# Optimization experiments

Hardware: AMD Instinct MI355X
Metric: run time of the kernel (lower is better)

## Reference

```python
import jax, jax.numpy as jnp
import numpy as np

B, E, F_IN = 8192, 64, 7
D, H = 64, 4           # feature_size, heads
HD = D // H            # features per head


def setup_inputs() -> dict:
    key = jax.random.key(0)
    ks = jax.random.split(key, 14)
    def lin(k, i, o):
        return jax.random.normal(k, (i, o), jnp.float32) * (1.0 / np.sqrt(i))
    return {
        "x": jax.random.normal(ks[0], (B, E, F_IN), jnp.float32),
        # ego embedding MLP (7->64->64, with bias)
        "ego_w0": lin(ks[1], F_IN, D), "ego_b0": jnp.zeros((D,), jnp.float32),
        "ego_w1": lin(ks[2], D, D),    "ego_b1": jnp.zeros((D,), jnp.float32),
        # others embedding MLP (separate weights)
        "oth_w0": lin(ks[3], F_IN, D), "oth_b0": jnp.zeros((D,), jnp.float32),
        "oth_w1": lin(ks[4], D, D),    "oth_b1": jnp.zeros((D,), jnp.float32),
        # attention projections (no bias)
        "Wk": lin(ks[5], D, D), "Wv": lin(ks[6], D, D),
        "Wq": lin(ks[7], D, D), "Wc": lin(ks[8], D, D),
    }


def _mlp(x, w0, b0, w1, b1):
    h = jax.nn.relu(x @ w0 + b0)
    return jax.nn.relu(h @ w1 + b1)


def reference(x, ego_w0, ego_b0, ego_w1, ego_b1,
              oth_w0, oth_b0, oth_w1, oth_b1, Wk, Wv, Wq, Wc):
    b = x.shape[0]
    mask = x[:, :, 0] < 0.5                       # [B, E] absent entities
    ego = _mlp(x[:, 0:1, :], ego_w0, ego_b0, ego_w1, ego_b1)   # [B, 1, D]
    others = _mlp(x[:, 1:, :], oth_w0, oth_b0, oth_w1, oth_b1)  # [B, E-1, D]
    input_all = jnp.concatenate([ego, others], axis=1)          # [B, E, D]

    # project and split heads -> [B, H, E, HD]
    k = (input_all @ Wk).reshape(b, E, H, HD).transpose(0, 2, 1, 3)
    v = (input_all @ Wv).reshape(b, E, H, HD).transpose(0, 2, 1, 3)
    q = (ego @ Wq).reshape(b, 1, H, HD).transpose(0, 2, 1, 3)   # [B, H, 1, HD]

    scores = jnp.einsum('bhqd,bhkd->bhqk', q, k) / np.sqrt(HD)  # [B, H, 1, E]
    scores = jnp.where(mask[:, None, None, :], -1e9, scores)
    p_attn = jax.nn.softmax(scores, axis=-1)
    out = jnp.einsum('bhqk,bhkd->bhqd', p_attn, v)              # [B, H, 1, HD]
    out = out.reshape(b, D)                                      # concat heads
    result = (out @ Wc + ego[:, 0, :]) * 0.5                     # [B, D]
    return result
```

## Files before the change

kernel.cpp:

```cpp
#include <hip/hip_runtime.h>
#include <hip/hip_bf16.h>


typedef __attribute__((ext_vector_type(8))) short short8;
typedef __attribute__((ext_vector_type(4))) short short4b;
typedef __attribute__((ext_vector_type(4))) float f32x4;

#define SY 72

#define LDS_FENCE() asm volatile("s_waitcnt lgkmcnt(0)" ::: "memory")

#define WS_G    0
#define WS_EGW0 16384
#define WS_EGW1 16896
#define WS_WVT  20992
#define WS_WCT  25088
#define WS_W0T  29184
#define WS_W1T  29696

__device__ __forceinline__ short f2bs(float x) {
    __hip_bfloat16 h = __float2bfloat16(x);
    return __builtin_bit_cast(short, h);
}
__device__ __forceinline__ unsigned short f2u(float x) {
    __hip_bfloat16 h = __float2bfloat16(x);
    return __builtin_bit_cast(unsigned short, h);
}
__device__ __forceinline__ short8 ldws8(const unsigned short* p) {
    return *(const short8*)p;
}

__global__ void pack_ws(const float* __restrict__ ego_w0, const float* __restrict__ ego_w1,
                        const float* __restrict__ oth_w0, const float* __restrict__ oth_w1,
                        const float* __restrict__ Wk, const float* __restrict__ Wv,
                        const float* __restrict__ Wq, const float* __restrict__ Wc,
                        unsigned short* __restrict__ ws) {
    const int blk = blockIdx.x, t = threadIdx.x;
    if (blk < 256) {
        const int n = blk, h = n >> 6, f = n & 63, j = t;
        float a = 0.f;
#pragma unroll
        for (int d = 0; d < 16; ++d)
            a = fmaf(Wq[j * 64 + h * 16 + d], Wk[f * 64 + h * 16 + d], a);
        ws[WS_G + n * 64 + j] = f2u(a);
    } else {
        const int n = blk - 256, k = t;
        ws[WS_EGW1 + n * 64 + k] = f2u(ego_w1[k * 64 + n]);
        ws[WS_WVT  + n * 64 + k] = f2u(Wv[k * 64 + n]);
        ws[WS_WCT  + n * 64 + k] = f2u(Wc[k * 64 + n]);
        ws[WS_W1T  + n * 64 + k] = f2u(oth_w1[k * 64 + n]);
        if (k < 8) {
            ws[WS_EGW0 + n * 8 + k] = (k < 7) ? f2u(ego_w0[k * 64 + n]) : 0;
            ws[WS_W0T  + n * 8 + k] = (k < 7) ? f2u(oth_w0[k * 64 + n]) : 0;
        }
    }
}

__global__ __launch_bounds__(64, 2)
void ego_attn_kernel(const float* __restrict__ x,
                     const float* __restrict__ ego_b0, const float* __restrict__ ego_b1,
                     const float* __restrict__ oth_b0, const float* __restrict__ oth_b1,
                     const unsigned short* __restrict__ ws,
                     float* __restrict__ out)
{
    __shared__ __align__(16) short hy[64 * SY];
    __shared__ __align__(16) short kqb[16 * SY];
    __shared__ __align__(16) short pa[4 * SY];
    __shared__ __align__(16) short py[16 * SY];
    __shared__ __align__(16) short xld[4 * 64 * 8];
    __shared__ __align__(16) float egf[4 * 64];
    __shared__ unsigned long long mball[4];

    const int lane = threadIdx.x;
    const int lg = lane >> 4, ln = lane & 15;
    const int gb = blockIdx.x * 4;
    const short8 z8 = {0, 0, 0, 0, 0, 0, 0, 0};

    short8 w0f[4], w1f[2][4];
#pragma unroll
    for (int ct = 0; ct < 4; ++ct)
        w0f[ct] = (lg == 0) ? ldws8(ws + WS_W0T + (ct * 16 + ln) * 8) : z8;
#pragma unroll
    for (int kc = 0; kc < 2; ++kc)
#pragma unroll
        for (int ct = 0; ct < 4; ++ct)
            w1f[kc][ct] = ldws8(ws + WS_W1T + (ct * 16 + ln) * 64 + kc * 32 + lg * 8);
    float b0v[4], b1v[4], eb0v[4], eb1v[4];
#pragma unroll
    for (int ct = 0; ct < 4; ++ct) {
        b0v[ct]  = oth_b0[ct * 16 + ln];
        b1v[ct]  = oth_b1[ct * 16 + ln];
        eb0v[ct] = ego_b0[ct * 16 + ln];
        eb1v[ct] = ego_b1[ct * 16 + ln];
    }

#pragma unroll
    for (int i = 0; i < 4; ++i) {
        const float* xr = x + (size_t)(gb + i) * 448 + lane * 7;
        const float v0 = xr[0];
        const unsigned long long mb = __ballot(v0 < 0.5f);
        if (lane == 0) mball[i] = mb;
        short8 v;
        v[0] = f2bs(v0);
#pragma unroll
        for (int k = 1; k < 7; ++k) v[k] = f2bs(xr[k]);
        v[7] = 0;
        *(short8*)&xld[((i << 6) | lane) * 8] = v;
    }
    LDS_FENCE();

    short8 xea;
    {
        const short8 t = *(const short8*)&xld[((ln & 3) << 6) * 8];
        xea = (lg == 0 && ln < 4) ? t : z8;
    }
#pragma unroll
    for (int ct = 0; ct < 4; ++ct) {
        const short8 bfr = (lg == 0) ? ldws8(ws + WS_EGW0 + (ct * 16 + ln) * 8) : z8;
        f32x4 c = {eb0v[ct], eb0v[ct], eb0v[ct], eb0v[ct]};
        c = __builtin_amdgcn_mfma_f32_16x16x32_bf16(xea, bfr, c, 0, 0, 0);
        if (lg == 0) {
#pragma unroll
            for (int r = 0; r < 4; ++r)
                hy[r * SY + ct * 16 + ln] = f2bs(fmaxf(c[r], 0.f));
        }
    }
    LDS_FENCE();
    short8 ha[2];
#pragma unroll
    for (int kc = 0; kc < 2; ++kc)
        ha[kc] = *(const short8*)&hy[(ln & 3) * SY + kc * 32 + lg * 8];
    LDS_FENCE();
#pragma unroll
    for (int ct = 0; ct < 4; ++ct) {
        f32x4 c = {eb1v[ct], eb1v[ct], eb1v[ct], eb1v[ct]};
#pragma unroll
        for (int kc = 0; kc < 2; ++kc) {
            const short8 bfr = ldws8(ws + WS_EGW1 + (ct * 16 + ln) * 64 + kc * 32 + lg * 8);
            c = __builtin_amdgcn_mfma_f32_16x16x32_bf16(ha[kc], bfr, c, 0, 0, 0);
        }
        if (lg == 0) {
#pragma unroll
            for (int r = 0; r < 4; ++r) {
                const float e = fmaxf(c[r], 0.f);
                egf[r * 64 + ct * 16 + ln] = e;
                hy[r * SY + ct * 16 + ln] = f2bs(e);
            }
        }
    }
    LDS_FENCE();
    short8 ea[2];
#pragma unroll
    for (int kc = 0; kc < 2; ++kc)
        ea[kc] = *(const short8*)&hy[(ln & 3) * SY + kc * 32 + lg * 8];

#pragma unroll 4
    for (int ctg = 0; ctg < 16; ++ctg) {
        f32x4 c = {0.f, 0.f, 0.f, 0.f};
#pragma unroll
        for (int kc = 0; kc < 2; ++kc) {
            const short8 bfr = ldws8(ws + WS_G + (ctg * 16 + ln) * 64 + kc * 32 + lg * 8);
            c = __builtin_amdgcn_mfma_f32_16x16x32_bf16(ea[kc], bfr, c, 0, 0, 0);
        }
        if (lg == 0) {
            const int h = ctg >> 2, fc = (ctg & 3) * 16 + ln;
#pragma unroll
            for (int r = 0; r < 4; ++r)
                kqb[(r * 4 + h) * SY + fc] = f2bs(c[r] * 0.25f);
        }
    }
    LDS_FENCE();

#pragma unroll 1
    for (int i = 0; i < 4; ++i) {
        short8 xa[4];
#pragma unroll
        for (int mt = 0; mt < 4; ++mt) {
            const short8 t = *(const short8*)&xld[((i << 6) | (mt * 16 + ln)) * 8];
            xa[mt] = (lg == 0) ? t : z8;
        }
        const unsigned long long mb = mball[i];

#pragma unroll
        for (int mt = 0; mt < 4; ++mt)
#pragma unroll
            for (int ct = 0; ct < 4; ++ct) {
                f32x4 c = {b0v[ct], b0v[ct], b0v[ct], b0v[ct]};
                c = __builtin_amdgcn_mfma_f32_16x16x32_bf16(xa[mt], w0f[ct], c, 0, 0, 0);
#pragma unroll
                for (int r = 0; r < 4; ++r)
                    hy[(mt * 16 + lg * 4 + r) * SY + ct * 16 + ln] = f2bs(fmaxf(c[r], 0.f));
            }
        LDS_FENCE();
        short8 a2[4][2];
#pragma unroll
        for (int mt = 0; mt < 4; ++mt)
#pragma unroll
            for (int kc = 0; kc < 2; ++kc)
                a2[mt][kc] = *(const short8*)&hy[(mt * 16 + ln) * SY + kc * 32 + lg * 8];
        LDS_FENCE();
#pragma unroll
        for (int ct = 0; ct < 4; ++ct)
#pragma unroll
            for (int mt = 0; mt < 4; ++mt) {
                f32x4 c = {b1v[ct], b1v[ct], b1v[ct], b1v[ct]};
                c = __builtin_amdgcn_mfma_f32_16x16x32_bf16(a2[mt][0], w1f[0][ct], c, 0, 0, 0);
                c = __builtin_amdgcn_mfma_f32_16x16x32_bf16(a2[mt][1], w1f[1][ct], c, 0, 0, 0);
#pragma unroll
                for (int r = 0; r < 4; ++r)
                    hy[(mt * 16 + lg * 4 + r) * SY + ct * 16 + ln] = f2bs(fmaxf(c[r], 0.f));
            }
        if (lg == 0) {
#pragma unroll
            for (int ct = 0; ct < 4; ++ct)
                hy[ct * 16 + ln] = f2bs(egf[i * 64 + ct * 16 + ln]);
        }
        LDS_FENCE();
        short8 kb[2];
#pragma unroll
        for (int kc = 0; kc < 2; ++kc)
            kb[kc] = *(const short8*)&kqb[(i * 4 + (ln & 3)) * SY + kc * 32 + lg * 8];

        float sv[16];
        float m = -3e38f;
#pragma unroll
        for (int mt = 0; mt < 4; ++mt) {
            const short8 ya0 = *(const short8*)&hy[(mt * 16 + ln) * SY + 0 * 32 + lg * 8];
            const short8 ya1 = *(const short8*)&hy[(mt * 16 + ln) * SY + 1 * 32 + lg * 8];
            f32x4 c = {0.f, 0.f, 0.f, 0.f};
            c = __builtin_amdgcn_mfma_f32_16x16x32_bf16(ya0, kb[0], c, 0, 0, 0);
            c = __builtin_amdgcn_mfma_f32_16x16x32_bf16(ya1, kb[1], c, 0, 0, 0);
#pragma unroll
            for (int r = 0; r < 4; ++r) {
                float s = c[r];
                if ((mb >> (mt * 16 + lg * 4 + r)) & 1ull) s = -1e9f;
                sv[mt * 4 + r] = s;
                m = fmaxf(m, s);
            }
        }
        m = fmaxf(m, __shfl_xor(m, 16));
        m = fmaxf(m, __shfl_xor(m, 32));
        float sum = 0.f;
#pragma unroll
        for (int k = 0; k < 16; ++k) { sv[k] = __expf(sv[k] - m); sum += sv[k]; }
        sum += __shfl_xor(sum, 16);
        sum += __shfl_xor(sum, 32);
        const float inv = 1.f / sum;
        if (ln < 4) {
#pragma unroll
            for (int mt = 0; mt < 4; ++mt) {
                short4b pk;
#pragma unroll
                for (int r = 0; r < 4; ++r) pk[r] = f2bs(sv[mt * 4 + r] * inv);
                *(short4b*)&pa[ln * SY + mt * 16 + lg * 4] = pk;
            }
        }
        LDS_FENCE();
        short8 pf[2];
#pragma unroll
        for (int kc = 0; kc < 2; ++kc)
            pf[kc] = *(const short8*)&pa[(ln & 3) * SY + kc * 32 + lg * 8];
#pragma unroll
        for (int ct = 0; ct < 4; ++ct) {
            f32x4 c = {0.f, 0.f, 0.f, 0.f};
#pragma unroll
            for (int kc = 0; kc < 2; ++kc) {
                short8 yv;
#pragma unroll
                for (int j = 0; j < 8; ++j)
                    yv[j] = hy[(kc * 32 + lg * 8 + j) * SY + ct * 16 + ln];
                c = __builtin_amdgcn_mfma_f32_16x16x32_bf16(pf[kc], yv, c, 0, 0, 0);
            }
            if (lg == 0) {
#pragma unroll
                for (int r = 0; r < 4; ++r)
                    py[(r * 4 + i) * SY + ct * 16 + ln] = f2bs(c[r]);
            }
        }
        LDS_FENCE();
    }

#pragma unroll
    for (int ct = 0; ct < 4; ++ct) {
        short8 af[2];
#pragma unroll
        for (int kc = 0; kc < 2; ++kc)
            af[kc] = *(const short8*)&py[(ct * 4 + (ln & 3)) * SY + kc * 32 + lg * 8];
        f32x4 c = {0.f, 0.f, 0.f, 0.f};
#pragma unroll
        for (int kc = 0; kc < 2; ++kc) {
            const short8 bfr = ldws8(ws + WS_WVT + (ct * 16 + ln) * 64 + kc * 32 + lg * 8);
            c = __builtin_amdgcn_mfma_f32_16x16x32_bf16(af[kc], bfr, c, 0, 0, 0);
        }
        if (lg == 0) {
#pragma unroll
            for (int r = 0; r < 4; ++r)
                hy[r * SY + ct * 16 + ln] = f2bs(c[r]);
        }
    }
    LDS_FENCE();
    short8 oa[2];
#pragma unroll
    for (int kc = 0; kc < 2; ++kc)
        oa[kc] = *(const short8*)&hy[(ln & 3) * SY + kc * 32 + lg * 8];
#pragma unroll
    for (int ct = 0; ct < 4; ++ct) {
        f32x4 c = {0.f, 0.f, 0.f, 0.f};
#pragma unroll
        for (int kc = 0; kc < 2; ++kc) {
            const short8 bfr = ldws8(ws + WS_WCT + (ct * 16 + ln) * 64 + kc * 32 + lg * 8);
            c = __builtin_amdgcn_mfma_f32_16x16x32_bf16(oa[kc], bfr, c, 0, 0, 0);
        }
        if (lg == 0) {
#pragma unroll
            for (int r = 0; r < 4; ++r)
                out[(size_t)(gb + r) * 64 + ct * 16 + ln] = (c[r] + egf[r * 64 + ct * 16 + ln]) * 0.5f;
        }
    }
}

extern "C" void kernel_launch(void* const* d_in, const int* in_sizes, int n_in,
                              void* d_out, int out_size, void* d_ws, size_t ws_size,
                              hipStream_t stream) {
    const float* x      = (const float*)d_in[0];
    const float* ego_w0 = (const float*)d_in[1];
    const float* ego_b0 = (const float*)d_in[2];
    const float* ego_w1 = (const float*)d_in[3];
    const float* ego_b1 = (const float*)d_in[4];
    const float* oth_w0 = (const float*)d_in[5];
    const float* oth_b0 = (const float*)d_in[6];
    const float* oth_w1 = (const float*)d_in[7];
    const float* oth_b1 = (const float*)d_in[8];
    const float* Wk     = (const float*)d_in[9];
    const float* Wv     = (const float*)d_in[10];
    const float* Wq     = (const float*)d_in[11];
    const float* Wc     = (const float*)d_in[12];

    unsigned short* ws = (unsigned short*)d_ws;
    pack_ws<<<320, 64, 0, stream>>>(ego_w0, ego_w1, oth_w0, oth_w1,
                                    Wk, Wv, Wq, Wc, ws);
    ego_attn_kernel<<<2048, 64, 0, stream>>>(
        x, ego_b0, ego_b1, oth_b0, oth_b1, ws, (float*)d_out);
}
```

Baseline: 121.5 us.

## Process eight batch rows per block and transpose MFMA operands for packed stores

Each block now handles 8 batch rows instead of 4, halving the grid. The cost of per-block weight register loads and the ego/query projection MFMAs is spread over more rows, and the MFMA padding waste in the M dimension drops from 4 of 16 rows to 8 of 16. Several MFMAs swap their A and B operands so the outputs land in row-major order, which allows packed 4-wide bf16 LDS stores and float4 bias loads. In exchange the per-row entity loop becomes serial over 8 iterations per block, so there are fewer blocks to hide latency and parallelism drops (1024 single-wave blocks).

After: 125.9 us. +3.6%, slower.

```diff
diff --git a/kernel.cpp b/kernel.cpp
--- a/kernel.cpp
+++ b/kernel.cpp
@@ -28,6 +28,18 @@
 }
 __device__ __forceinline__ short8 ldws8(const unsigned short* p) {
     return *(const short8*)p;
+}
+__device__ __forceinline__ short4b pk4r(f32x4 c) {
+    short4b p;
+#pragma unroll
+    for (int r = 0; r < 4; ++r) p[r] = f2bs(fmaxf(c[r], 0.f));
+    return p;
+}
+__device__ __forceinline__ short4b pk4s(f32x4 c, float s) {
+    short4b p;
+#pragma unroll
+    for (int r = 0; r < 4; ++r) p[r] = f2bs(c[r] * s);
+    return p;
 }
 
 __global__ void pack_ws(const float* __restrict__ ego_w0, const float* __restrict__ ego_w1,
@@ -64,38 +76,33 @@
                      float* __restrict__ out)
 {
     __shared__ __align__(16) short hy[64 * SY];
-    __shared__ __align__(16) short kqb[16 * SY];
+    __shared__ __align__(16) short kqb[32 * SY];
     __shared__ __align__(16) short pa[4 * SY];
-    __shared__ __align__(16) short py[16 * SY];
-    __shared__ __align__(16) short xld[4 * 64 * 8];
-    __shared__ __align__(16) float egf[4 * 64];
-    __shared__ unsigned long long mball[4];
+    __shared__ __align__(16) short py[32 * SY];
+    __shared__ __align__(16) short xld[8 * 64 * 8];
+    __shared__ __align__(16) float egf[8 * 64];
+    __shared__ unsigned long long mball[8];
 
     const int lane = threadIdx.x;
     const int lg = lane >> 4, ln = lane & 15;
-    const int gb = blockIdx.x * 4;
+    const int gb = blockIdx.x * 8;
     const short8 z8 = {0, 0, 0, 0, 0, 0, 0, 0};
 
     short8 w0f[4], w1f[2][4];
 #pragma unroll
-    for (int ct = 0; ct < 4; ++ct)
-        w0f[ct] = (lg == 0) ? ldws8(ws + WS_W0T + (ct * 16 + ln) * 8) : z8;
+    for (int t = 0; t < 4; ++t)
+        w0f[t] = (lg == 0) ? ldws8(ws + WS_W0T + (t * 16 + ln) * 8) : z8;
 #pragma unroll
     for (int kc = 0; kc < 2; ++kc)
 #pragma unroll
-        for (int ct = 0; ct < 4; ++ct)
-            w1f[kc][ct] = ldws8(ws + WS_W1T + (ct * 16 + ln) * 64 + kc * 32 + lg * 8);
-    float b0v[4], b1v[4], eb0v[4], eb1v[4];
-#pragma unroll
-    for (int ct = 0; ct < 4; ++ct) {
-        b0v[ct]  = oth_b0[ct * 16 + ln];
-        b1v[ct]  = oth_b1[ct * 16 + ln];
-        eb0v[ct] = ego_b0[ct * 16 + ln];
-        eb1v[ct] = ego_b1[ct * 16 + ln];
-    }
-
-#pragma unroll
-    for (int i = 0; i < 4; ++i) {
+        for (int t = 0; t < 4; ++t)
+            w1f[kc][t] = ldws8(ws + WS_W1T + (t * 16 + ln) * 64 + kc * 32 + lg * 8);
+    float eb1v[4];
+#pragma unroll
+    for (int t = 0; t < 4; ++t) eb1v[t] = ego_b1[t * 16 + ln];
+
+#pragma unroll
+    for (int i = 0; i < 8; ++i) {
         const float* xr = x + (size_t)(gb + i) * 448 + lane * 7;
         const float v0 = xr[0];
         const unsigned long long mb = __ballot(v0 < 0.5f);
@@ -111,25 +118,23 @@
 
     short8 xea;
     {
-        const short8 t = *(const short8*)&xld[((ln & 3) << 6) * 8];
-        xea = (lg == 0 && ln < 4) ? t : z8;
-    }
-#pragma unroll
-    for (int ct = 0; ct < 4; ++ct) {
-        const short8 bfr = (lg == 0) ? ldws8(ws + WS_EGW0 + (ct * 16 + ln) * 8) : z8;
-        f32x4 c = {eb0v[ct], eb0v[ct], eb0v[ct], eb0v[ct]};
-        c = __builtin_amdgcn_mfma_f32_16x16x32_bf16(xea, bfr, c, 0, 0, 0);
-        if (lg == 0) {
-#pragma unroll
-            for (int r = 0; r < 4; ++r)
-                hy[r * SY + ct * 16 + ln] = f2bs(fmaxf(c[r], 0.f));
-        }
+        const short8 t = *(const short8*)&xld[((ln & 7) << 6) * 8];
+        xea = (lg == 0 && ln < 8) ? t : z8;
+    }
+#pragma unroll
+    for (int dt = 0; dt < 4; ++dt) {
+        const short8 af = (lg == 0) ? ldws8(ws + WS_EGW0 + (dt * 16 + ln) * 8) : z8;
+        const float4 bq = *(const float4*)&ego_b0[dt * 16 + lg * 4];
+        f32x4 c = {bq.x, bq.y, bq.z, bq.w};
+        c = __builtin_amdgcn_mfma_f32_16x16x32_bf16(af, xea, c, 0, 0, 0);
+        if (ln < 8)
+            *(short4b*)&hy[ln * SY + dt * 16 + lg * 4] = pk4r(c);
     }
     LDS_FENCE();
     short8 ha[2];
 #pragma unroll
     for (int kc = 0; kc < 2; ++kc)
-        ha[kc] = *(const short8*)&hy[(ln & 3) * SY + kc * 32 + lg * 8];
+        ha[kc] = *(const short8*)&hy[(ln & 7) * SY + kc * 32 + lg * 8];
     LDS_FENCE();
 #pragma unroll
     for (int ct = 0; ct < 4; ++ct) {
@@ -139,12 +144,12 @@
             const short8 bfr = ldws8(ws + WS_EGW1 + (ct * 16 + ln) * 64 + kc * 32 + lg * 8);
             c = __builtin_amdgcn_mfma_f32_16x16x32_bf16(ha[kc], bfr, c, 0, 0, 0);
         }
-        if (lg == 0) {
+        if (lg < 2) {
 #pragma unroll
             for (int r = 0; r < 4; ++r) {
                 const float e = fmaxf(c[r], 0.f);
-                egf[r * 64 + ct * 16 + ln] = e;
-                hy[r * SY + ct * 16 + ln] = f2bs(e);
+                egf[(lg * 4 + r) * 64 + ct * 16 + ln] = e;
+                hy[(lg * 4 + r) * SY + ct * 16 + ln] = f2bs(e);
             }
         }
     }
@@ -152,27 +157,24 @@
     short8 ea[2];
 #pragma unroll
     for (int kc = 0; kc < 2; ++kc)
-        ea[kc] = *(const short8*)&hy[(ln & 3) * SY + kc * 32 + lg * 8];
+        ea[kc] = *(const short8*)&hy[(ln & 7) * SY + kc * 32 + lg * 8];
 
 #pragma unroll 4
     for (int ctg = 0; ctg < 16; ++ctg) {
         f32x4 c = {0.f, 0.f, 0.f, 0.f};
 #pragma unroll
         for (int kc = 0; kc < 2; ++kc) {
-            const short8 bfr = ldws8(ws + WS_G + (ctg * 16 + ln) * 64 + kc * 32 + lg * 8);
-            c = __builtin_amdgcn_mfma_f32_16x16x32_bf16(ea[kc], bfr, c, 0, 0, 0);
-        }
-        if (lg == 0) {
-            const int h = ctg >> 2, fc = (ctg & 3) * 16 + ln;
-#pragma unroll
-            for (int r = 0; r < 4; ++r)
-                kqb[(r * 4 + h) * SY + fc] = f2bs(c[r] * 0.25f);
-        }
+            const short8 g = ldws8(ws + WS_G + (ctg * 16 + ln) * 64 + kc * 32 + lg * 8);
+            c = __builtin_amdgcn_mfma_f32_16x16x32_bf16(g, ea[kc], c, 0, 0, 0);
+        }
+        if (ln < 8)
+            *(short4b*)&kqb[(ln * 4 + (ctg >> 2)) * SY + (ctg & 3) * 16 + lg * 4] =
+                pk4s(c, 0.25f);
     }
     LDS_FENCE();
 
 #pragma unroll 1
-    for (int i = 0; i < 4; ++i) {
+    for (int i = 0; i < 8; ++i) {
         short8 xa[4];
 #pragma unroll
         for (int mt = 0; mt < 4; ++mt) {
@@ -182,15 +184,15 @@
         const unsigned long long mb = mball[i];
 
 #pragma unroll
-        for (int mt = 0; mt < 4; ++mt)
-#pragma unroll
-            for (int ct = 0; ct < 4; ++ct) {
-                f32x4 c = {b0v[ct], b0v[ct], b0v[ct], b0v[ct]};
-                c = __builtin_amdgcn_mfma_f32_16x16x32_bf16(xa[mt], w0f[ct], c, 0, 0, 0);
-#pragma unroll
-                for (int r = 0; r < 4; ++r)
-                    hy[(mt * 16 + lg * 4 + r) * SY + ct * 16 + ln] = f2bs(fmaxf(c[r], 0.f));
-            }
+        for (int dt = 0; dt < 4; ++dt) {
+            const float4 bq = *(const float4*)&oth_b0[dt * 16 + lg * 4];
+#pragma unroll
+            for (int et = 0; et < 4; ++et) {
+                f32x4 c = {bq.x, bq.y, bq.z, bq.w};
+                c = __builtin_amdgcn_mfma_f32_16x16x32_bf16(w0f[dt], xa[et], c, 0, 0, 0);
+                *(short4b*)&hy[(et * 16 + ln) * SY + dt * 16 + lg * 4] = pk4r(c);
+            }
+        }
         LDS_FENCE();
         short8 a2[4][2];
 #pragma unroll
@@ -200,16 +202,16 @@
                 a2[mt][kc] = *(const short8*)&hy[(mt * 16 + ln) * SY + kc * 32 + lg * 8];
         LDS_FENCE();
 #pragma unroll
-        for (int ct = 0; ct < 4; ++ct)
-#pragma unroll
-            for (int mt = 0; mt < 4; ++mt) {
-                f32x4 c = {b1v[ct], b1v[ct], b1v[ct], b1v[ct]};
-                c = __builtin_amdgcn_mfma_f32_16x16x32_bf16(a2[mt][0], w1f[0][ct], c, 0, 0, 0);
-                c = __builtin_amdgcn_mfma_f32_16x16x32_bf16(a2[mt][1], w1f[1][ct], c, 0, 0, 0);
-#pragma unroll
-                for (int r = 0; r < 4; ++r)
-                    hy[(mt * 16 + lg * 4 + r) * SY + ct * 16 + ln] = f2bs(fmaxf(c[r], 0.f));
-            }
+        for (int dt = 0; dt < 4; ++dt) {
+            const float4 bq = *(const float4*)&oth_b1[dt * 16 + lg * 4];
+#pragma unroll
+            for (int et = 0; et < 4; ++et) {
+                f32x4 c = {bq.x, bq.y, bq.z, bq.w};
+                c = __builtin_amdgcn_mfma_f32_16x16x32_bf16(w1f[0][dt], a2[et][0], c, 0, 0, 0);
+                c = __builtin_amdgcn_mfma_f32_16x16x32_bf16(w1f[1][dt], a2[et][1], c, 0, 0, 0);
+                *(short4b*)&hy[(et * 16 + ln) * SY + dt * 16 + lg * 4] = pk4r(c);
+            }
+        }
         if (lg == 0) {
 #pragma unroll
             for (int ct = 0; ct < 4; ++ct)
@@ -274,7 +276,7 @@
             if (lg == 0) {
 #pragma unroll
                 for (int r = 0; r < 4; ++r)
-                    py[(r * 4 + i) * SY + ct * 16 + ln] = f2bs(c[r]);
+                    py[(r * 8 + i) * SY + ct * 16 + ln] = f2bs(c[r]);
             }
         }
         LDS_FENCE();
@@ -285,24 +287,24 @@
         short8 af[2];
 #pragma unroll
         for (int kc = 0; kc < 2; ++kc)
-            af[kc] = *(const short8*)&py[(ct * 4 + (ln & 3)) * SY + kc * 32 + lg * 8];
+            af[kc] = *(const short8*)&py[(ct * 8 + (ln & 7)) * SY + kc * 32 + lg * 8];
         f32x4 c = {0.f, 0.f, 0.f, 0.f};
 #pragma unroll
         for (int kc = 0; kc < 2; ++kc) {
             const short8 bfr = ldws8(ws + WS_WVT + (ct * 16 + ln) * 64 + kc * 32 + lg * 8);
             c = __builtin_amdgcn_mfma_f32_16x16x32_bf16(af[kc], bfr, c, 0, 0, 0);
         }
-        if (lg == 0) {
+        if (lg < 2) {
 #pragma unroll
             for (int r = 0; r < 4; ++r)
-                hy[r * SY + ct * 16 + ln] = f2bs(c[r]);
+                hy[(lg * 4 + r) * SY + ct * 16 + ln] = f2bs(c[r]);
         }
     }
     LDS_FENCE();
     short8 oa[2];
 #pragma unroll
     for (int kc = 0; kc < 2; ++kc)
-        oa[kc] = *(const short8*)&hy[(ln & 3) * SY + kc * 32 + lg * 8];
+        oa[kc] = *(const short8*)&hy[(ln & 7) * SY + kc * 32 + lg * 8];
 #pragma unroll
     for (int ct = 0; ct < 4; ++ct) {
         f32x4 c = {0.f, 0.f, 0.f, 0.f};
@@ -311,10 +313,11 @@
             const short8 bfr = ldws8(ws + WS_WCT + (ct * 16 + ln) * 64 + kc * 32 + lg * 8);
             c = __builtin_amdgcn_mfma_f32_16x16x32_bf16(oa[kc], bfr, c, 0, 0, 0);
         }
-        if (lg == 0) {
+        if (lg < 2) {
 #pragma unroll
             for (int r = 0; r < 4; ++r)
-                out[(size_t)(gb + r) * 64 + ct * 16 + ln] = (c[r] + egf[r * 64 + ct * 16 + ln]) * 0.5f;
+                out[(size_t)(gb + lg * 4 + r) * 64 + ct * 16 + ln] =
+                    (c[r] + egf[(lg * 4 + r) * 64 + ct * 16 + ln]) * 0.5f;
         }
     }
 }
@@ -339,6 +342,6 @@
     unsigned short* ws = (unsigned short*)d_ws;
     pack_ws<<<320, 64, 0, stream>>>(ego_w0, ego_w1, oth_w0, oth_w1,
                                     Wk, Wv, Wq, Wc, ws);
-    ego_attn_kernel<<<2048, 64, 0, stream>>>(
+    ego_attn_kernel<<<1024, 64, 0, stream>>>(
         x, ego_b0, ego_b1, oth_b0, oth_b1, ws, (float*)d_out);
 }
```
